# Kernel optimization log

Hardware: AMD Instinct MI355X
Metric: run time of the kernel (lower is better)

## Reference

```python
import jax, jax.numpy as jnp
import numpy as np
import math

B, T, C, H = 4, 2048, 1024, 16

def setup_inputs() -> dict:
    key = jax.random.key(0)
    ks = jax.random.split(key, 9)
    s = 0.02
    return {
        "x":  jax.random.normal(ks[0], (B, T, C), dtype=jnp.float32),
        "Wq": jax.random.normal(ks[1], (C, C), dtype=jnp.float32) * s,
        "bq": jax.random.normal(ks[2], (C,), dtype=jnp.float32) * s,
        "Wk": jax.random.normal(ks[3], (C, C), dtype=jnp.float32) * s,
        "bk": jax.random.normal(ks[4], (C,), dtype=jnp.float32) * s,
        "Wv": jax.random.normal(ks[5], (C, C), dtype=jnp.float32) * s,
        "bv": jax.random.normal(ks[6], (C,), dtype=jnp.float32) * s,
        "Wp": jax.random.normal(ks[7], (C, C), dtype=jnp.float32) * s,
        "bp": jax.random.normal(ks[8], (C,), dtype=jnp.float32) * s,
    }

def reference(x, Wq, bq, Wk, bk, Wv, bv, Wp, bp):
    b, t, c = x.shape
    h = H
    d = c // h
    # torch Linear: y = x @ W.T + b
    q = (x @ Wq.T + bq).reshape(b, t, h, d).transpose(0, 2, 1, 3)  # [B,H,T,d]
    k = (x @ Wk.T + bk).reshape(b, t, h, d).transpose(0, 2, 1, 3)
    v = (x @ Wv.T + bv).reshape(b, t, h, d).transpose(0, 2, 1, 3)
    att = jnp.einsum('bhqd,bhkd->bhqk', q, k) * (1.0 / math.sqrt(d))  # [B,H,T,T]
    causal = jnp.tril(jnp.ones((t, t), dtype=bool))
    att = jnp.where(causal[None, None, :, :], att, -jnp.inf)
    att = jax.nn.softmax(att, axis=-1)
    # attn_drop / resid_drop are identity in eval mode
    y = jnp.einsum('bhqk,bhkd->bhqd', att, v)        # [B,H,T,d]
    y = y.transpose(0, 2, 1, 3).reshape(b, t, c)      # [B,T,C]
    y = y @ Wp.T + bp
    return y
```

## Files before the change

kernel.cpp:

```cpp
#include <hip/hip_runtime.h>
#include <hip/hip_bf16.h>

typedef __attribute__((ext_vector_type(8))) short bf16x8;
typedef __attribute__((ext_vector_type(4))) float f32x4;

struct bf16x8_s { __hip_bfloat16 h[8]; };
struct bf16x4_s { __hip_bfloat16 h[4]; };

__global__ void cvt_kernel(const float* __restrict__ in,
                           __hip_bfloat16* __restrict__ out, int n8) {
  int i = blockIdx.x * blockDim.x + threadIdx.x;
  if (i >= n8) return;
  const float4* p = reinterpret_cast<const float4*>(in) + (size_t)i * 2;
  float4 a = p[0], b = p[1];
  bf16x8_s o;
  o.h[0] = __float2bfloat16(a.x); o.h[1] = __float2bfloat16(a.y);
  o.h[2] = __float2bfloat16(a.z); o.h[3] = __float2bfloat16(a.w);
  o.h[4] = __float2bfloat16(b.x); o.h[5] = __float2bfloat16(b.y);
  o.h[6] = __float2bfloat16(b.z); o.h[7] = __float2bfloat16(b.w);
  *reinterpret_cast<bf16x8_s*>(out + (size_t)i * 8) = o;
}

__global__ void cvt4_kernel(const float* __restrict__ w0,
                            const float* __restrict__ w1,
                            const float* __restrict__ w2,
                            const float* __restrict__ w3,
                            __hip_bfloat16* __restrict__ out) {
  const int bid = blockIdx.x;
  const int seg = bid >> 9;
  const int i = (bid & 511) * 256 + threadIdx.x;
  const float* src = seg == 0 ? w0 : seg == 1 ? w1 : seg == 2 ? w2 : w3;
  const float4* p = reinterpret_cast<const float4*>(src) + (size_t)i * 2;
  float4 a = p[0], b = p[1];
  bf16x8_s o;
  o.h[0] = __float2bfloat16(a.x); o.h[1] = __float2bfloat16(a.y);
  o.h[2] = __float2bfloat16(a.z); o.h[3] = __float2bfloat16(a.w);
  o.h[4] = __float2bfloat16(b.x); o.h[5] = __float2bfloat16(b.y);
  o.h[6] = __float2bfloat16(b.z); o.h[7] = __float2bfloat16(b.w);
  *reinterpret_cast<bf16x8_s*>(out + (size_t)seg * 1048576 + (size_t)i * 8) = o;
}

__device__ __forceinline__ void stage_tile(const __hip_bfloat16* src,
                                           char* lds, int tid) {
#pragma unroll
  for (int s = 0; s < 4; ++s) {
    const int c = s * 256 + tid;
    const int row = c >> 3;
    const int cb = (((c & 7) << 4) ^ ((row & 7) << 4));
    __builtin_amdgcn_global_load_lds(
        (const __attribute__((address_space(1))) void*)((const char*)(src + (size_t)row * 1024) + cb),
        (__attribute__((address_space(3))) void*)(lds + s * 4096 + (tid & 192) * 16),
        16, 0, 0);
  }
}

template <int MODE>
__global__ __launch_bounds__(256) void gemm128(
    const __hip_bfloat16* __restrict__ A, const __hip_bfloat16* __restrict__ W,
    const float* __restrict__ b0, const float* __restrict__ b1,
    const float* __restrict__ b2, void* __restrict__ O0,
    void* __restrict__ O1, void* __restrict__ O2) {
  constexpr float SC = 0.18033688011112042f;
  __shared__ char smem[32768];
  const int tid = threadIdx.x;
  const int lane = tid & 63;
  const int lrow = lane & 15;
  const int lhi = lane >> 4;
  const int wid = tid >> 6;
  const int wm = wid >> 1, wn = wid & 1;
  const int xr = (lrow & 7) << 4;

  const int n = blockIdx.x;
  const int wg = MODE == 0 ? (n & 7) * 192 + (n >> 3) : (n & 7) * 64 + (n >> 3);
  const int tm = wg & 63;
  const int tn = wg >> 6;
  const int row0 = tm * 128;

  const __hip_bfloat16* Ap = A + (size_t)row0 * 1024;
  const __hip_bfloat16* Wp = W + (size_t)(tn * 128) * 1024;

  f32x4 acc[4][4] = {};

  for (int k0 = 0; k0 < 1024; k0 += 64) {
    stage_tile(Ap + k0, smem, tid);
    stage_tile(Wp + k0, smem + 16384, tid);
    __syncthreads();
    bf16x8 af[4][2], bfr[4][2];
#pragma unroll
    for (int m = 0; m < 4; ++m) {
      const int ar = wm * 64 + m * 16 + lrow;
#pragma unroll
      for (int kk = 0; kk < 2; ++kk)
        af[m][kk] = *reinterpret_cast<const bf16x8*>(
            smem + ar * 128 + ((kk * 64 + lhi * 16) ^ xr));
    }
#pragma unroll
    for (int nn = 0; nn < 4; ++nn) {
      const int br = wn * 64 + nn * 16 + lrow;
#pragma unroll
      for (int kk = 0; kk < 2; ++kk)
        bfr[nn][kk] = *reinterpret_cast<const bf16x8*>(
            smem + 16384 + br * 128 + ((kk * 64 + lhi * 16) ^ xr));
    }
    __builtin_amdgcn_s_setprio(1);
#pragma unroll
    for (int kk = 0; kk < 2; ++kk)
#pragma unroll
      for (int m = 0; m < 4; ++m)
#pragma unroll
        for (int nn = 0; nn < 4; ++nn)
          acc[m][nn] = __builtin_amdgcn_mfma_f32_16x16x32_bf16(
              af[m][kk], bfr[nn][kk], acc[m][nn], 0, 0, 0);
    __builtin_amdgcn_s_setprio(0);
    __syncthreads();
  }

  char* epi = smem + wid * 8192;
  const int grow0 = row0 + wm * 64;

  if constexpr (MODE == 0) {
    const int sel = tn >> 3;
    const int cloc = (tn & 7) * 128 + wn * 64;
    const float* bias = sel == 0 ? b0 : sel == 1 ? b1 : b2;
    float bv4[4];
#pragma unroll
    for (int nn = 0; nn < 4; ++nn) bv4[nn] = bias[cloc + nn * 16 + lrow];

    if (sel != 2) {
      __hip_bfloat16* dst = sel == 0 ? (__hip_bfloat16*)O0 : (__hip_bfloat16*)O1;
#pragma unroll
      for (int mg = 0; mg < 4; ++mg) {
#pragma unroll
        for (int nn = 0; nn < 4; ++nn)
#pragma unroll
          for (int i = 0; i < 4; ++i) {
            float v = acc[mg][nn][i] + bv4[nn];
            if (sel == 0) v *= SC;
            ((__hip_bfloat16*)epi)[(lhi * 4 + i) * 72 + nn * 16 + lrow] =
                __float2bfloat16(v);
          }
#pragma unroll
        for (int ps = 0; ps < 2; ++ps) {
          const int r = ps * 8 + (lane >> 3);
          bf16x8 val = *reinterpret_cast<const bf16x8*>(epi + r * 144 + (lane & 7) * 16);
          const int grow = grow0 + mg * 16 + r;
          *reinterpret_cast<bf16x8*>(&dst[(size_t)grow * 1024 + cloc + (lane & 7) * 8]) = val;
        }
      }
    } else {
      __hip_bfloat16* dst = (__hip_bfloat16*)O2;
      const int h = cloc >> 6;
      const int bb = grow0 >> 11;
      const int t0 = grow0 & 2047;
      __hip_bfloat16* vb = dst + ((size_t)(bb * 16 + h) * 64) * 2048;
#pragma unroll
      for (int ng = 0; ng < 4; ++ng) {
#pragma unroll
        for (int m = 0; m < 4; ++m)
#pragma unroll
          for (int i = 0; i < 4; ++i) {
            const float v = acc[m][ng][i] + bv4[ng];
            ((__hip_bfloat16*)epi)[lrow * 72 + m * 16 + lhi * 4 + i] =
                __float2bfloat16(v);
          }
#pragma unroll
        for (int ps = 0; ps < 2; ++ps) {
          const int dr = ps * 8 + (lane >> 3);
          bf16x8 val = *reinterpret_cast<const bf16x8*>(epi + dr * 144 + (lane & 7) * 16);
          const int d = ng * 16 + dr;
          *reinterpret_cast<bf16x8*>(&vb[(size_t)d * 2048 + t0 + (lane & 7) * 8]) = val;
        }
      }
    }
  } else {
    float* dst = (float*)O0;
    const int cloc = tn * 128 + wn * 64;
    float bv4[4];
#pragma unroll
    for (int nn = 0; nn < 4; ++nn) bv4[nn] = b0[cloc + nn * 16 + lrow];
#pragma unroll
    for (int mg = 0; mg < 4; ++mg) {
#pragma unroll
      for (int nn = 0; nn < 4; ++nn)
#pragma unroll
        for (int i = 0; i < 4; ++i)
          ((float*)epi)[(lhi * 4 + i) * 68 + nn * 16 + lrow] =
              acc[mg][nn][i] + bv4[nn];
#pragma unroll
      for (int ps = 0; ps < 4; ++ps) {
        const int r = ps * 4 + (lane >> 4);
        float4 val = *reinterpret_cast<const float4*>(epi + r * 272 + (lane & 15) * 16);
        const int grow = grow0 + mg * 16 + r;
        *reinterpret_cast<float4*>(&dst[(size_t)grow * 1024 + cloc + (lane & 15) * 4]) = val;
      }
    }
  }
}

__device__ __forceinline__ void stage_kv(char* __restrict__ smem, int buf,
                                         const __hip_bfloat16* __restrict__ Kb,
                                         const __hip_bfloat16* __restrict__ Vb,
                                         int kv0, int tid) {
  const int w = tid >> 6, l = tid & 63;
  char* base = smem + buf * 16384;
#pragma unroll
  for (int s = 0; s < 2; ++s) {
    const int c = s * 256 + w * 64 + l;
    const int row = c >> 3;
    const int scb = ((c & 7) << 4) ^ ((row & 7) << 4);
    __builtin_amdgcn_global_load_lds(
        (const __attribute__((address_space(1))) void*)(Kb + (size_t)(kv0 + row) * 1024 + (scb >> 1)),
        (__attribute__((address_space(3))) void*)(base + s * 4096 + w * 1024), 16, 0, 0);
  }
#pragma unroll
  for (int s = 0; s < 2; ++s) {
    const int c = s * 256 + w * 64 + l;
    const int row = c >> 3;
    const int scb = ((c & 7) << 4) ^ ((row & 7) << 4);
    __builtin_amdgcn_global_load_lds(
        (const __attribute__((address_space(1))) void*)(Vb + (size_t)row * 2048 + kv0 + (scb >> 1)),
        (__attribute__((address_space(3))) void*)(base + 8192 + s * 4096 + w * 1024), 16, 0, 0);
  }
}

template <bool MASKED>
__device__ __forceinline__ void attn_step(
    int kv0, int q0, int lrow, int lhi, const char* __restrict__ kvb,
    const bf16x8 qf[2], f32x4 o[4], float& m, float& l,
    char* __restrict__ Pw) {
  constexpr float TH = 8.0f;
  const int xr = (lrow & 7) << 4;
  f32x4 s[4] = {};
  __builtin_amdgcn_s_setprio(1);
#pragma unroll
  for (int g = 0; g < 4; ++g) {
    const char* rowp = kvb + (g * 16 + lrow) * 128;
#pragma unroll
    for (int kk = 0; kk < 2; ++kk) {
      bf16x8 kf = *reinterpret_cast<const bf16x8*>(rowp + ((kk * 64 + lhi * 16) ^ xr));
      s[g] = __builtin_amdgcn_mfma_f32_16x16x32_bf16(kf, qf[kk], s[g], 0, 0, 0);
    }
  }
  __builtin_amdgcn_s_setprio(0);
  if (MASKED) {
#pragma unroll
    for (int g = 0; g < 4; ++g)
#pragma unroll
      for (int i = 0; i < 4; ++i) {
        const int k = kv0 + g * 16 + lhi * 4 + i;
        if (k > q0 + lrow) s[g][i] = -1e30f;
      }
  }
  float gm[4];
#pragma unroll
  for (int g = 0; g < 4; ++g)
    gm[g] = fmaxf(fmaxf(s[g][0], s[g][1]), fmaxf(s[g][2], s[g][3]));
  float mx = fmaxf(fmaxf(gm[0], gm[1]), fmaxf(gm[2], gm[3]));
  mx = fmaxf(mx, __shfl_xor(mx, 16));
  mx = fmaxf(mx, __shfl_xor(mx, 32));
  if (__any(mx > m + TH)) {
    const float nm = fmaxf(m, mx);
    const float al = exp2f(m - nm);
    m = nm;
    l *= al;
    float a4[4];
#pragma unroll
    for (int i = 0; i < 4; ++i) a4[i] = __shfl(al, 4 * lhi + i, 16);
#pragma unroll
    for (int f = 0; f < 4; ++f)
#pragma unroll
      for (int i = 0; i < 4; ++i) o[f][i] *= a4[i];
  }
  float gs[4];
#pragma unroll
  for (int g = 0; g < 4; ++g) {
    bf16x4_s t4;
    float p0 = exp2f(s[g][0] - m);
    float p1 = exp2f(s[g][1] - m);
    float p2 = exp2f(s[g][2] - m);
    float p3 = exp2f(s[g][3] - m);
    t4.h[0] = __float2bfloat16(p0); t4.h[1] = __float2bfloat16(p1);
    t4.h[2] = __float2bfloat16(p2); t4.h[3] = __float2bfloat16(p3);
    gs[g] = (p0 + p1) + (p2 + p3);
    *reinterpret_cast<bf16x4_s*>(Pw + lrow * 128 + ((g * 32 + lhi * 8) ^ xr)) = t4;
  }
  float sum = (gs[0] + gs[1]) + (gs[2] + gs[3]);
  sum += __shfl_xor(sum, 16);
  sum += __shfl_xor(sum, 32);
  l += sum;
  bf16x8 pf[2];
#pragma unroll
  for (int nn = 0; nn < 2; ++nn)
    pf[nn] = *reinterpret_cast<const bf16x8*>(
        Pw + lrow * 128 + ((nn * 64 + lhi * 16) ^ xr));
  __builtin_amdgcn_s_setprio(1);
#pragma unroll
  for (int nn = 0; nn < 2; ++nn)
#pragma unroll
    for (int f = 0; f < 4; ++f) {
      bf16x8 vf = *reinterpret_cast<const bf16x8*>(
          kvb + 8192 + (f * 16 + lrow) * 128 + ((nn * 64 + lhi * 16) ^ xr));
      o[f] = __builtin_amdgcn_mfma_f32_16x16x32_bf16(pf[nn], vf, o[f], 0, 0, 0);
    }
  __builtin_amdgcn_s_setprio(0);
}

__global__ __launch_bounds__(256, 4) void attn_fwd(
    const __hip_bfloat16* __restrict__ Q, const __hip_bfloat16* __restrict__ Km,
    const __hip_bfloat16* __restrict__ Vt, __hip_bfloat16* __restrict__ Y) {
  constexpr int T = 2048, C = 1024, D = 64;
  const int tid = threadIdx.x;
  const int wid = tid >> 6;
  const int lane = tid & 63;
  const int lrow = lane & 15;
  const int lhi = lane >> 4;
  const int n = blockIdx.x;
  const int xcd = n & 7;
  const int w8 = n >> 3;
  const int bh = xcd * 8 + (w8 & 7);
  const int qt = 31 - (w8 >> 3);
  const int b = bh >> 4, h = bh & 15;
  const int q0 = qt * 64 + wid * 16;

  const __hip_bfloat16* Qb = Q + ((size_t)b * T) * C + h * D;
  const __hip_bfloat16* Kb = Km + ((size_t)b * T) * C + h * D;
  const __hip_bfloat16* Vb = Vt + (size_t)bh * D * T;

  __shared__ char smem[40960];
  char* Pw = smem + 32768 + wid * 2048;

  bf16x8 qf[2];
#pragma unroll
  for (int kk = 0; kk < 2; ++kk)
    qf[kk] = *reinterpret_cast<const bf16x8*>(
        Qb + (size_t)(q0 + lrow) * C + kk * 32 + lhi * 8);

  f32x4 o[4] = {};
  float m = -1e30f, l = 0.f;

  const int nt = qt + 1;

  stage_kv(smem, 0, Kb, Vb, 0, tid);
  for (int t = 0; t < nt; ++t) {
    __syncthreads();
    if (t + 1 < nt) stage_kv(smem, (t + 1) & 1, Kb, Vb, (t + 1) * 64, tid);
    const char* kvb = smem + (t & 1) * 16384;
    if (t == nt - 1)
      attn_step<true>(t * 64, q0, lrow, lhi, kvb, qf, o, m, l, Pw);
    else
      attn_step<false>(t * 64, q0, lrow, lhi, kvb, qf, o, m, l, Pw);
  }

  float l4[4];
#pragma unroll
  for (int i = 0; i < 4; ++i) l4[i] = __shfl(l, 4 * lhi + i, 16);
#pragma unroll
  for (int f = 0; f < 4; ++f)
#pragma unroll
    for (int i = 0; i < 4; ++i) {
      const int row = q0 + 4 * lhi + i;
      Y[((size_t)b * T + row) * C + h * D + f * 16 + lrow] =
          __float2bfloat16(o[f][i] / l4[i]);
    }
}

extern "C" void kernel_launch(void* const* d_in, const int* in_sizes, int n_in,
                              void* d_out, int out_size, void* d_ws,
                              size_t ws_size, hipStream_t stream) {
  const float* x = (const float*)d_in[0];
  const float* Wq = (const float*)d_in[1];
  const float* bq = (const float*)d_in[2];
  const float* Wk = (const float*)d_in[3];
  const float* bk = (const float*)d_in[4];
  const float* Wv = (const float*)d_in[5];
  const float* bv = (const float*)d_in[6];
  const float* Wp = (const float*)d_in[7];
  const float* bp = (const float*)d_in[8];
  float* out = (float*)d_out;

  __hip_bfloat16* ws = (__hip_bfloat16*)d_ws;
  __hip_bfloat16* xb = ws;
  __hip_bfloat16* wqb = xb + 8388608;
  __hip_bfloat16* wpb = wqb + 3 * 1048576;
  __hip_bfloat16* Qs = wqb + 4 * 1048576;
  __hip_bfloat16* Ks = Qs + 8388608;
  __hip_bfloat16* Vts = Ks + 8388608;
  __hip_bfloat16* Ys = Vts + 8388608;

  cvt_kernel<<<4096, 256, 0, stream>>>(x, xb, 1048576);
  cvt4_kernel<<<2048, 256, 0, stream>>>(Wq, Wk, Wv, Wp, wqb);

  gemm128<0><<<dim3(1536), 256, 0, stream>>>(xb, wqb, bq, bk, bv, Qs, Ks, Vts);

  attn_fwd<<<dim3(2048), 256, 0, stream>>>(Qs, Ks, Vts, Ys);

  gemm128<1><<<dim3(512), 256, 0, stream>>>(Ys, wpb, bp, nullptr, nullptr, out,
                                            nullptr, nullptr);
}
```

Before: 182.2 us.

## Switch attention to 32x32x16 MFMA with register-only P via permlane32 swap

Rewrites the attention inner step to use 32x32x16 bf16 MFMAs with 32 query rows per wave and 128-row query tiles per block, halving the grid. Instead of round-tripping the softmax probabilities through LDS, P is packed with v_cvt_pk_bf16_f32 and rearranged with v_permlane32_swap into the A-operand layout directly in registers. This is meant to remove the LDS store/load of P and improve MFMA efficiency and K/V reuse, at the cost of more registers per thread (launch bounds occupancy hint dropped) and coarser causal load balancing, since waves in a block finish at different kv tiles.

After: 192.3 us. 5.6% more time.

```diff
diff --git a/kernel.cpp b/kernel.cpp
--- a/kernel.cpp
+++ b/kernel.cpp
@@ -3,9 +3,10 @@
 
 typedef __attribute__((ext_vector_type(8))) short bf16x8;
 typedef __attribute__((ext_vector_type(4))) float f32x4;
+typedef __attribute__((ext_vector_type(16))) float f32x16;
 
 struct bf16x8_s { __hip_bfloat16 h[8]; };
-struct bf16x4_s { __hip_bfloat16 h[4]; };
+struct int4_s { int d[4]; };
 
 __global__ void cvt_kernel(const float* __restrict__ in,
                            __hip_bfloat16* __restrict__ out, int n8) {
@@ -225,143 +226,155 @@
 
 template <bool MASKED>
 __device__ __forceinline__ void attn_step(
-    int kv0, int q0, int lrow, int lhi, const char* __restrict__ kvb,
-    const bf16x8 qf[2], f32x4 o[4], float& m, float& l,
-    char* __restrict__ Pw) {
+    int kv0, int q0w, int lane, const char* __restrict__ kvb,
+    const bf16x8 qf[4], f32x16 o[2], float& m, float& l) {
   constexpr float TH = 8.0f;
-  const int xr = (lrow & 7) << 4;
-  f32x4 s[4] = {};
+  const int q = lane & 31;
+  const int hi = lane >> 5;
+  const int xr = (lane & 7) << 4;
+  f32x16 s[2] = {};
   __builtin_amdgcn_s_setprio(1);
 #pragma unroll
-  for (int g = 0; g < 4; ++g) {
-    const char* rowp = kvb + (g * 16 + lrow) * 128;
-#pragma unroll
-    for (int kk = 0; kk < 2; ++kk) {
-      bf16x8 kf = *reinterpret_cast<const bf16x8*>(rowp + ((kk * 64 + lhi * 16) ^ xr));
-      s[g] = __builtin_amdgcn_mfma_f32_16x16x32_bf16(kf, qf[kk], s[g], 0, 0, 0);
+  for (int kvb2 = 0; kvb2 < 2; ++kvb2) {
+    const char* rowp = kvb + (kvb2 * 32 + q) * 128;
+#pragma unroll
+    for (int dk = 0; dk < 4; ++dk) {
+      bf16x8 kA = *reinterpret_cast<const bf16x8*>(rowp + ((dk * 32 + hi * 16) ^ xr));
+      s[kvb2] = __builtin_amdgcn_mfma_f32_32x32x16_bf16(kA, qf[dk], s[kvb2], 0, 0, 0);
     }
   }
   __builtin_amdgcn_s_setprio(0);
   if (MASKED) {
 #pragma unroll
-    for (int g = 0; g < 4; ++g)
-#pragma unroll
-      for (int i = 0; i < 4; ++i) {
-        const int k = kv0 + g * 16 + lhi * 4 + i;
-        if (k > q0 + lrow) s[g][i] = -1e30f;
+    for (int kvb2 = 0; kvb2 < 2; ++kvb2)
+#pragma unroll
+      for (int r = 0; r < 16; ++r) {
+        const int kv = kv0 + kvb2 * 32 + (r & 3) + 8 * (r >> 2) + 4 * hi;
+        if (kv > q0w + q) s[kvb2][r] = -1e30f;
       }
   }
-  float gm[4];
-#pragma unroll
-  for (int g = 0; g < 4; ++g)
-    gm[g] = fmaxf(fmaxf(s[g][0], s[g][1]), fmaxf(s[g][2], s[g][3]));
-  float mx = fmaxf(fmaxf(gm[0], gm[1]), fmaxf(gm[2], gm[3]));
-  mx = fmaxf(mx, __shfl_xor(mx, 16));
+  float v8[8];
+#pragma unroll
+  for (int u = 0; u < 8; ++u)
+    v8[u] = fmaxf(fmaxf(s[0][u], s[0][u + 8]), fmaxf(s[1][u], s[1][u + 8]));
+  float mx = fmaxf(fmaxf(fmaxf(v8[0], v8[1]), fmaxf(v8[2], v8[3])),
+                   fmaxf(fmaxf(v8[4], v8[5]), fmaxf(v8[6], v8[7])));
   mx = fmaxf(mx, __shfl_xor(mx, 32));
   if (__any(mx > m + TH)) {
     const float nm = fmaxf(m, mx);
     const float al = exp2f(m - nm);
     m = nm;
     l *= al;
-    float a4[4];
-#pragma unroll
-    for (int i = 0; i < 4; ++i) a4[i] = __shfl(al, 4 * lhi + i, 16);
-#pragma unroll
-    for (int f = 0; f < 4; ++f)
-#pragma unroll
-      for (int i = 0; i < 4; ++i) o[f][i] *= a4[i];
-  }
-  float gs[4];
-#pragma unroll
-  for (int g = 0; g < 4; ++g) {
-    bf16x4_s t4;
-    float p0 = exp2f(s[g][0] - m);
-    float p1 = exp2f(s[g][1] - m);
-    float p2 = exp2f(s[g][2] - m);
-    float p3 = exp2f(s[g][3] - m);
-    t4.h[0] = __float2bfloat16(p0); t4.h[1] = __float2bfloat16(p1);
-    t4.h[2] = __float2bfloat16(p2); t4.h[3] = __float2bfloat16(p3);
-    gs[g] = (p0 + p1) + (p2 + p3);
-    *reinterpret_cast<bf16x4_s*>(Pw + lrow * 128 + ((g * 32 + lhi * 8) ^ xr)) = t4;
-  }
-  float sum = (gs[0] + gs[1]) + (gs[2] + gs[3]);
-  sum += __shfl_xor(sum, 16);
+#pragma unroll
+    for (int r = 0; r < 16; ++r) {
+      const float ar = __shfl(al, (r & 3) + 8 * (r >> 2) + 4 * hi, 32);
+      o[0][r] *= ar;
+      o[1][r] *= ar;
+    }
+  }
+#pragma unroll
+  for (int kvb2 = 0; kvb2 < 2; ++kvb2)
+#pragma unroll
+    for (int r = 0; r < 16; ++r) s[kvb2][r] = exp2f(s[kvb2][r] - m);
+  float sv[8];
+#pragma unroll
+  for (int u = 0; u < 8; ++u)
+    sv[u] = (s[0][u] + s[0][u + 8]) + (s[1][u] + s[1][u + 8]);
+  float sum = ((sv[0] + sv[1]) + (sv[2] + sv[3])) + ((sv[4] + sv[5]) + (sv[6] + sv[7]));
   sum += __shfl_xor(sum, 32);
   l += sum;
-  bf16x8 pf[2];
-#pragma unroll
-  for (int nn = 0; nn < 2; ++nn)
-    pf[nn] = *reinterpret_cast<const bf16x8*>(
-        Pw + lrow * 128 + ((nn * 64 + lhi * 16) ^ xr));
+  int pk[2][8];
+#pragma unroll
+  for (int kvb2 = 0; kvb2 < 2; ++kvb2)
+#pragma unroll
+    for (int u = 0; u < 8; ++u)
+      asm("v_cvt_pk_bf16_f32 %0, %1, %2"
+          : "=v"(pk[kvb2][u])
+          : "v"(s[kvb2][2 * u]), "v"(s[kvb2][2 * u + 1]));
+  int4_s pa[4];
+#pragma unroll
+  for (int ks = 0; ks < 4; ++ks) {
+    const int kb = ks >> 1, u0 = (ks & 1) * 4;
+    int d0 = pk[kb][u0 + 0], d2 = pk[kb][u0 + 2];
+    asm("v_permlane32_swap_b32 %0, %1" : "+v"(d0), "+v"(d2));
+    int d1 = pk[kb][u0 + 1], d3 = pk[kb][u0 + 3];
+    asm("v_permlane32_swap_b32 %0, %1" : "+v"(d1), "+v"(d3));
+    pa[ks].d[0] = d0;
+    pa[ks].d[1] = d1;
+    pa[ks].d[2] = d2;
+    pa[ks].d[3] = d3;
+  }
   __builtin_amdgcn_s_setprio(1);
 #pragma unroll
-  for (int nn = 0; nn < 2; ++nn)
-#pragma unroll
-    for (int f = 0; f < 4; ++f) {
-      bf16x8 vf = *reinterpret_cast<const bf16x8*>(
-          kvb + 8192 + (f * 16 + lrow) * 128 + ((nn * 64 + lhi * 16) ^ xr));
-      o[f] = __builtin_amdgcn_mfma_f32_16x16x32_bf16(pf[nn], vf, o[f], 0, 0, 0);
-    }
+  for (int d0b = 0; d0b < 2; ++d0b) {
+    const char* vrow = kvb + 8192 + (d0b * 32 + q) * 128;
+#pragma unroll
+    for (int ks = 0; ks < 4; ++ks) {
+      bf16x8 vf = *reinterpret_cast<const bf16x8*>(vrow + ((ks * 32 + hi * 16) ^ xr));
+      o[d0b] = __builtin_amdgcn_mfma_f32_32x32x16_bf16(
+          *reinterpret_cast<const bf16x8*>(&pa[ks]), vf, o[d0b], 0, 0, 0);
+    }
+  }
   __builtin_amdgcn_s_setprio(0);
 }
 
-__global__ __launch_bounds__(256, 4) void attn_fwd(
+__global__ __launch_bounds__(256) void attn_fwd(
     const __hip_bfloat16* __restrict__ Q, const __hip_bfloat16* __restrict__ Km,
     const __hip_bfloat16* __restrict__ Vt, __hip_bfloat16* __restrict__ Y) {
   constexpr int T = 2048, C = 1024, D = 64;
   const int tid = threadIdx.x;
   const int wid = tid >> 6;
   const int lane = tid & 63;
-  const int lrow = lane & 15;
-  const int lhi = lane >> 4;
+  const int q = lane & 31;
+  const int hi = lane >> 5;
   const int n = blockIdx.x;
   const int xcd = n & 7;
   const int w8 = n >> 3;
   const int bh = xcd * 8 + (w8 & 7);
-  const int qt = 31 - (w8 >> 3);
+  const int qt = 15 - (w8 >> 3);
   const int b = bh >> 4, h = bh & 15;
-  const int q0 = qt * 64 + wid * 16;
+  const int q0w = qt * 128 + wid * 32;
 
   const __hip_bfloat16* Qb = Q + ((size_t)b * T) * C + h * D;
   const __hip_bfloat16* Kb = Km + ((size_t)b * T) * C + h * D;
   const __hip_bfloat16* Vb = Vt + (size_t)bh * D * T;
 
-  __shared__ char smem[40960];
-  char* Pw = smem + 32768 + wid * 2048;
-
-  bf16x8 qf[2];
-#pragma unroll
-  for (int kk = 0; kk < 2; ++kk)
-    qf[kk] = *reinterpret_cast<const bf16x8*>(
-        Qb + (size_t)(q0 + lrow) * C + kk * 32 + lhi * 8);
-
-  f32x4 o[4] = {};
+  __shared__ char smem[32768];
+
+  bf16x8 qf[4];
+#pragma unroll
+  for (int dk = 0; dk < 4; ++dk)
+    qf[dk] = *reinterpret_cast<const bf16x8*>(
+        Qb + (size_t)(q0w + q) * C + dk * 16 + hi * 8);
+
+  f32x16 o[2] = {};
   float m = -1e30f, l = 0.f;
 
-  const int nt = qt + 1;
+  const int nt = 2 * qt + 2;
+  const int ns = (q0w >> 6) + 1;
 
   stage_kv(smem, 0, Kb, Vb, 0, tid);
   for (int t = 0; t < nt; ++t) {
     __syncthreads();
     if (t + 1 < nt) stage_kv(smem, (t + 1) & 1, Kb, Vb, (t + 1) * 64, tid);
-    const char* kvb = smem + (t & 1) * 16384;
-    if (t == nt - 1)
-      attn_step<true>(t * 64, q0, lrow, lhi, kvb, qf, o, m, l, Pw);
-    else
-      attn_step<false>(t * 64, q0, lrow, lhi, kvb, qf, o, m, l, Pw);
-  }
-
-  float l4[4];
-#pragma unroll
-  for (int i = 0; i < 4; ++i) l4[i] = __shfl(l, 4 * lhi + i, 16);
-#pragma unroll
-  for (int f = 0; f < 4; ++f)
-#pragma unroll
-    for (int i = 0; i < 4; ++i) {
-      const int row = q0 + 4 * lhi + i;
-      Y[((size_t)b * T + row) * C + h * D + f * 16 + lrow] =
-          __float2bfloat16(o[f][i] / l4[i]);
-    }
+    if (t < ns) {
+      const char* kvb = smem + (t & 1) * 16384;
+      if (t == ns - 1)
+        attn_step<true>(t * 64, q0w, lane, kvb, qf, o, m, l);
+      else
+        attn_step<false>(t * 64, q0w, lane, kvb, qf, o, m, l);
+    }
+  }
+
+#pragma unroll
+  for (int r = 0; r < 16; ++r) {
+    const float lr = __shfl(l, (r & 3) + 8 * (r >> 2) + 4 * hi, 32);
+    const float inv = 1.0f / lr;
+    const int row = q0w + (r & 3) + 8 * (r >> 2) + 4 * hi;
+    __hip_bfloat16* yp = Y + ((size_t)b * T + row) * C + h * D + q;
+    yp[0] = __float2bfloat16(o[0][r] * inv);
+    yp[32] = __float2bfloat16(o[1][r] * inv);
+  }
 }
 
 extern "C" void kernel_launch(void* const* d_in, const int* in_sizes, int n_in,
@@ -392,7 +405,7 @@
 
   gemm128<0><<<dim3(1536), 256, 0, stream>>>(xb, wqb, bq, bk, bv, Qs, Ks, Vts);
 
-  attn_fwd<<<dim3(2048), 256, 0, stream>>>(Qs, Ks, Vts, Ys);
+  attn_fwd<<<dim3(1024), 256, 0, stream>>>(Qs, Ks, Vts, Ys);
 
   gemm128<1><<<dim3(512), 256, 0, stream>>>(Ys, wpb, bp, nullptr, nullptr, out,
                                             nullptr, nullptr);
```
